# Optimization experiments

Measured on AMD Instinct MI355X. Metric: run time of the kernel, lower is better.

The kernel has to match this reference:

```python
import jax, jax.numpy as jnp
import numpy as np

B, S, HID = 1, 2048, 4096
NH, NKV, HD = 32, 8, 128
N_REP = NH // NKV
SCALING = HD ** -0.5
NEG_INF = jnp.float32(-jnp.inf)


def rotate_half(x):
    x1, x2 = jnp.split(x, 2, axis=-1)
    return jnp.concatenate((-x2, x1), axis=-1)


def setup_inputs() -> dict:
    key = jax.random.key(0)
    ks = jax.random.split(key, 8)
    hidden_states = jax.random.normal(ks[0], (B, S, HID), dtype=jnp.float32)
    # RoPE tables (uniform stand-ins; real cos/sin come from rotary embedding)
    pos = jnp.arange(S, dtype=jnp.float32)[:, None]
    inv_freq = 1.0 / (10000.0 ** (jnp.arange(0, HD, 2, dtype=jnp.float32) / HD))
    ang = pos * inv_freq[None, :]              # [S, HD/2]
    emb = jnp.concatenate([ang, ang], axis=-1)  # [S, HD]
    cos = jnp.cos(emb)[None].repeat(B, axis=0)  # [B, S, HD]
    sin = jnp.sin(emb)[None].repeat(B, axis=0)
    # HF-style additive causal mask: 0 on/below diagonal, -inf above
    tril = jnp.tril(jnp.ones((S, S), dtype=bool))
    attention_mask = jnp.where(tril, 0.0, NEG_INF).astype(jnp.float32)[None, None]  # [B,1,S,S]
    scale = 0.02
    q_w = jax.random.normal(ks[1], (HID, HID), dtype=jnp.float32) * scale
    k_w = jax.random.normal(ks[2], (NKV * HD, HID), dtype=jnp.float32) * scale
    v_w = jax.random.normal(ks[3], (NKV * HD, HID), dtype=jnp.float32) * scale
    o_w = jax.random.normal(ks[4], (HID, HID), dtype=jnp.float32) * scale
    return {"hidden_states": hidden_states, "cos": cos, "sin": sin,
            "attention_mask": attention_mask, "q_w": q_w, "k_w": k_w,
            "v_w": v_w, "o_w": o_w}


def reference(hidden_states, cos, sin, attention_mask, q_w, k_w, v_w, o_w):
    b, s, _ = hidden_states.shape
    # projections -> [B, H, S, D]
    q = (hidden_states @ q_w.T).reshape(b, s, NH, HD).transpose(0, 2, 1, 3)
    k = (hidden_states @ k_w.T).reshape(b, s, NKV, HD).transpose(0, 2, 1, 3)
    v = (hidden_states @ v_w.T).reshape(b, s, NKV, HD).transpose(0, 2, 1, 3)
    # RoPE (unsqueeze_dim=1)
    cos_u = cos[:, None, :, :]
    sin_u = sin[:, None, :, :]
    q = q * cos_u + rotate_half(q) * sin_u
    k = k * cos_u + rotate_half(k) * sin_u
    # repeat_kv (interleave each kv head n_rep times)
    k = jnp.repeat(k, N_REP, axis=1)
    v = jnp.repeat(v, N_REP, axis=1)
    attn = jnp.einsum("bhqd,bhkd->bhqk", q, k)
    # gen_mask: 0 -> 1, -inf -> 0 (passthrough otherwise)
    m = attention_mask
    mask01 = jnp.where(m == 0, 1.0, jnp.where(jnp.isneginf(m), 0.0, m))
    attn = attn * mask01
    causal = m[:, :, :, : k.shape[-2]]
    attn = (attn + causal) * SCALING
    probs = jax.nn.softmax(attn.astype(jnp.float32), axis=-1).astype(q.dtype)
    # dropout p=attention_dropout=0.0 in eval -> identity
    ctx = jnp.einsum("bhqk,bhkd->bhqd", probs, v)  # [B,H,S,D]
    out = ctx.transpose(0, 2, 1, 3).reshape(b, s, -1) @ o_w.T
    return out
```

## Files before the change

### kernel.cpp

```cpp
#include <hip/hip_runtime.h>


typedef __attribute__((ext_vector_type(8))) short bf16x8;
typedef __attribute__((ext_vector_type(4))) float f32x4;
typedef __attribute__((ext_vector_type(4))) unsigned short u16x4;

#define S_LEN 2048
#define HID 4096
#define NH 32
#define NKV 8
#define HD 128
#define KVDIM 1024
#define SCALING 0.08838834764831845f

__device__ inline unsigned short f2bf(float f) {
  unsigned u = __builtin_bit_cast(unsigned, f);
  u = (u + 0x7FFFu + ((u >> 16) & 1u)) >> 16;
  return (unsigned short)u;
}
__device__ inline unsigned short f2bf_fast(float f) {
  unsigned u = __builtin_bit_cast(unsigned, f);
  return (unsigned short)((u + 0x8000u) >> 16);
}
__device__ inline float bf2f(unsigned short h) {
  unsigned u = ((unsigned)h) << 16;
  return __builtin_bit_cast(float, u);
}

__device__ inline void gload_lds16(const unsigned short* g, unsigned short* l) {
  __builtin_amdgcn_global_load_lds(
      (const __attribute__((address_space(1))) void*)g,
      (__attribute__((address_space(3))) void*)l, 16, 0, 0);
}

#define SZ_HS (8388608u)
#define SZ_QW (16777216u)
#define SZ_KW (4194304u)
#define B0 SZ_HS
#define B1 (B0 + SZ_QW)
#define B2 (B1 + SZ_KW)
#define B3 (B2 + SZ_KW)
#define B4 (B3 + SZ_QW)

__global__ void cvt_all(const float* __restrict__ s0,
                        const float* __restrict__ s1,
                        const float* __restrict__ s2,
                        const float* __restrict__ s3,
                        const float* __restrict__ s4,
                        unsigned short* __restrict__ dst) {
  size_t i = ((size_t)blockIdx.x * blockDim.x + threadIdx.x) * 4;
  const float* src;
  size_t off;
  if (i < B0)      { src = s0; off = i; }
  else if (i < B1) { src = s1; off = i - B0; }
  else if (i < B2) { src = s2; off = i - B1; }
  else if (i < B3) { src = s3; off = i - B2; }
  else             { src = s4; off = i - B3; }
  f32x4 v = *(const f32x4*)(src + off);
  u16x4 o;
#pragma unroll
  for (int r = 0; r < 4; ++r) o[r] = f2bf(v[r]);
  *(u16x4*)(dst + i) = o;
}

__global__ __launch_bounds__(256, 3) void gemm_qkv(
    const unsigned short* __restrict__ A, const unsigned short* __restrict__ Bq_,
    const unsigned short* __restrict__ Bk_, const unsigned short* __restrict__ Bv_,
    unsigned short* __restrict__ Cq, unsigned short* __restrict__ Ck,
    unsigned short* __restrict__ Cvt) {
  __shared__ unsigned short As[2][128 * 32];
  __shared__ unsigned short Bs[2][128 * 32];
  const int K = HID;
  const int tid = threadIdx.x;
  const int lane = tid & 63;
  const int wave = tid >> 6;
  const int orig = blockIdx.y * gridDim.x + blockIdx.x;
  const int xcd = orig & 7, seq = orig >> 3;
  const int xt = xcd * ((int)gridDim.x >> 3) + (seq >> 4);
  const int yt = seq & 15;
  const int m0 = yt * 128;
  const int wr = wave >> 1, wc = wave & 1;
  const int lrow = lane & 15, lg = lane >> 4;

  const unsigned short* Bsel;
  if (xt < 32)      Bsel = Bq_ + (size_t)(xt * 128) * K;
  else if (xt < 40) Bsel = Bk_ + (size_t)((xt - 32) * 128) * K;
  else              Bsel = Bv_ + (size_t)((xt - 40) * 128) * K;

  const f32x4 zero = {0.f, 0.f, 0.f, 0.f};
  f32x4 acc[4][4];
#pragma unroll
  for (int i = 0; i < 4; ++i)
#pragma unroll
    for (int j = 0; j < 4; ++j) acc[i][j] = zero;

  const int r0s = tid >> 2, c0s = (tid & 3) * 8;
  const int r1s = (tid + 256) >> 2, c1s = ((tid + 256) & 3) * 8;
  const unsigned short* Ag0 = A + (size_t)(m0 + r0s) * K + c0s;
  const unsigned short* Ag1 = A + (size_t)(m0 + r1s) * K + c1s;
  const unsigned short* Bg0 = Bsel + (size_t)r0s * K + c0s;
  const unsigned short* Bg1 = Bsel + (size_t)r1s * K + c1s;
  unsigned short* Al0[2] = {&As[0][tid * 8], &As[1][tid * 8]};
  unsigned short* Al1[2] = {&As[0][(tid + 256) * 8], &As[1][(tid + 256) * 8]};
  unsigned short* Bl0[2] = {&Bs[0][tid * 8], &Bs[1][tid * 8]};
  unsigned short* Bl1[2] = {&Bs[0][(tid + 256) * 8], &Bs[1][(tid + 256) * 8]};

#define QKV_STAGE(buf, koff)                                                  \
  {                                                                           \
    gload_lds16(Ag0 + (koff), Al0[buf]);                                      \
    gload_lds16(Ag1 + (koff), Al1[buf]);                                      \
    gload_lds16(Bg0 + (koff), Bl0[buf]);                                      \
    gload_lds16(Bg1 + (koff), Bl1[buf]);                                      \
  }

  QKV_STAGE(0, 0);
  __syncthreads();
  int cur = 0;
  const int NT = K >> 5;
  for (int kt = 0; kt < NT; ++kt) {
    if (kt + 1 < NT) QKV_STAGE(cur ^ 1, (kt + 1) * 32);
    bf16x8 af[4], bq[4];
#pragma unroll
    for (int i = 0; i < 4; ++i) {
      af[i] = *(const bf16x8*)(&As[cur][(wr * 64 + i * 16 + lrow) * 32 + lg * 8]);
      bq[i] = *(const bf16x8*)(&Bs[cur][(wc * 64 + i * 16 + lrow) * 32 + lg * 8]);
    }
#pragma unroll
    for (int i = 0; i < 4; ++i)
#pragma unroll
      for (int j = 0; j < 4; ++j)
        acc[i][j] = __builtin_amdgcn_mfma_f32_16x16x32_bf16(af[i], bq[j],
                                                            acc[i][j], 0, 0, 0);
    __syncthreads();
    cur ^= 1;
  }
#undef QKV_STAGE

  if (xt < 32) {
    const int n0 = xt * 128;
#pragma unroll
    for (int i = 0; i < 4; ++i)
#pragma unroll
      for (int j = 0; j < 4; ++j) {
        const int mm = m0 + wr * 64 + i * 16 + lg * 4;
        const int nn = n0 + wc * 64 + j * 16 + lrow;
#pragma unroll
        for (int r = 0; r < 4; ++r)
          Cq[(size_t)(mm + r) * HID + nn] = f2bf(acc[i][j][r]);
      }
  } else if (xt < 40) {
    const int n0 = (xt - 32) * 128;
#pragma unroll
    for (int i = 0; i < 4; ++i)
#pragma unroll
      for (int j = 0; j < 4; ++j) {
        const int mm = m0 + wr * 64 + i * 16 + lg * 4;
        const int nn = n0 + wc * 64 + j * 16 + lrow;
#pragma unroll
        for (int r = 0; r < 4; ++r)
          Ck[(size_t)(mm + r) * KVDIM + nn] = f2bf(acc[i][j][r]);
      }
  } else {
    const int n0 = (xt - 40) * 128;
#pragma unroll
    for (int i = 0; i < 4; ++i)
#pragma unroll
      for (int j = 0; j < 4; ++j) {
        const int mm = m0 + wr * 64 + i * 16 + lg * 4;
        const int nn = n0 + wc * 64 + j * 16 + lrow;
        u16x4 pk;
#pragma unroll
        for (int r = 0; r < 4; ++r) pk[r] = f2bf(acc[i][j][r]);
        *(u16x4*)(Cvt + (size_t)nn * S_LEN + mm) = pk;
      }
  }
}

#define GEMM_STAGE(Abase, Bbase, buf, koff)                                   \
  {                                                                           \
    _Pragma("unroll") for (int q = 0; q < 4; ++q)                             \
        gload_lds16(Abase + (size_t)(q * 32) * K + (koff), Asl[buf] + q * 2048); \
    _Pragma("unroll") for (int q = 0; q < 4; ++q)                             \
        gload_lds16(Bbase + (size_t)(q * 32) * K + (koff), Bsl[buf] + q * 2048); \
  }

#define GEMM_COMPUTE(cur)                                                     \
  {                                                                           \
    bf16x8 af[4][2], bq[4][2];                                                \
    const int r7 = lrow & 7;                                                  \
    _Pragma("unroll") for (int i = 0; i < 4; ++i) {                           \
      const int arow = wr * 64 + i * 16 + lrow;                               \
      const int brow = wc * 64 + i * 16 + lrow;                               \
      _Pragma("unroll") for (int ks = 0; ks < 2; ++ks) {                      \
        af[i][ks] = *(const bf16x8*)(As[cur] + arow * 64 +                    \
                                     (((ks * 4 + lg) ^ r7) * 8));             \
        bq[i][ks] = *(const bf16x8*)(Bs[cur] + brow * 64 +                    \
                                     (((ks * 4 + lg) ^ r7) * 8));             \
      }                                                                       \
    }                                                                         \
    _Pragma("unroll") for (int i = 0; i < 4; ++i)                             \
        _Pragma("unroll") for (int j = 0; j < 4; ++j) {                       \
      acc[i][j] = __builtin_amdgcn_mfma_f32_16x16x32_bf16(af[i][0], bq[j][0], \
                                                          acc[i][j], 0, 0, 0);\
      acc[i][j] = __builtin_amdgcn_mfma_f32_16x16x32_bf16(af[i][1], bq[j][1], \
                                                          acc[i][j], 0, 0, 0);\
    }                                                                         \
  }

__global__ __launch_bounds__(256, 2) void gemm_o(
    const unsigned short* __restrict__ A, const unsigned short* __restrict__ B,
    float* __restrict__ C) {
  __shared__ unsigned short As[2][128 * 64];
  __shared__ unsigned short Bs[2][128 * 64];
  const int K = HID;
  const int tid = threadIdx.x;
  const int lane = tid & 63;
  const int wave = tid >> 6;
  const int orig = blockIdx.y * gridDim.x + blockIdx.x;
  const int xcd = orig & 7, seq = orig >> 3;
  const int xt = xcd * ((int)gridDim.x >> 3) + (seq >> 4);
  const int yt = seq & 15;
  const int m0 = yt * 128;
  const int n0 = xt * 128;
  const int wr = wave >> 1, wc = wave & 1;
  const int lrow = lane & 15, lg = lane >> 4;

  const f32x4 zero = {0.f, 0.f, 0.f, 0.f};
  f32x4 acc[4][4];
#pragma unroll
  for (int i = 0; i < 4; ++i)
#pragma unroll
    for (int j = 0; j < 4; ++j) acc[i][j] = zero;

  const int srow = tid >> 3;
  const int scol = ((tid & 7) ^ (srow & 7)) * 8;
  const unsigned short* Agb = A + (size_t)(m0 + srow) * K + scol;
  const unsigned short* Bgb = B + (size_t)(n0 + srow) * K + scol;
  unsigned short* Asl[2] = {As[0] + tid * 8, As[1] + tid * 8};
  unsigned short* Bsl[2] = {Bs[0] + tid * 8, Bs[1] + tid * 8};

  GEMM_STAGE(Agb, Bgb, 0, 0);
  __syncthreads();
  int cur = 0;
  const int NT = K / 64;
  for (int kt = 0; kt < NT; ++kt) {
    if (kt + 1 < NT) GEMM_STAGE(Agb, Bgb, cur ^ 1, (kt + 1) * 64);
    GEMM_COMPUTE(cur);
    __syncthreads();
    cur ^= 1;
  }

#pragma unroll
  for (int i = 0; i < 4; ++i)
#pragma unroll
    for (int j = 0; j < 4; ++j) {
      const int mm = m0 + wr * 64 + i * 16 + lg * 4;
      const int nn = n0 + wc * 64 + j * 16 + lrow;
#pragma unroll
      for (int r = 0; r < 4; ++r)
        C[(size_t)(mm + r) * HID + nn] = acc[i][j][r];
    }
}

__global__ void rope_qk(unsigned short* __restrict__ q,
                        unsigned short* __restrict__ k,
                        const float* __restrict__ cosb,
                        const float* __restrict__ sinb) {
  const int s = blockIdx.x;
  const int t = threadIdx.x;
  unsigned short* x;
  int h, d4, rowstride;
  if (t < 512) { x = q; rowstride = HID;   h = t >> 4;        d4 = t & 15; }
  else         { x = k; rowstride = KVDIM; h = (t - 512) >> 4; d4 = (t - 512) & 15; }
  const int d = d4 * 4;
  const f32x4 c = *(const f32x4*)(cosb + s * 128 + d);
  const f32x4 sn = *(const f32x4*)(sinb + s * 128 + d);
  unsigned short* base = x + (size_t)s * rowstride + h * 128;
  u16x4 lo = *(u16x4*)(base + d);
  u16x4 hi = *(u16x4*)(base + d + 64);
  u16x4 olo, ohi;
#pragma unroll
  for (int r = 0; r < 4; ++r) {
    float lf = bf2f(lo[r]), hf = bf2f(hi[r]);
    olo[r] = f2bf(lf * c[r] - hf * sn[r]);
    ohi[r] = f2bf(hf * c[r] + lf * sn[r]);
  }
  *(u16x4*)(base + d) = olo;
  *(u16x4*)(base + d + 64) = ohi;
}

__global__ __launch_bounds__(256, 2) void attn_kernel(
    const unsigned short* __restrict__ Q, const unsigned short* __restrict__ Kc,
    const unsigned short* __restrict__ Vt, unsigned short* __restrict__ ctx) {
  __shared__ unsigned short Ks[64 * 128];
  __shared__ unsigned short Vs[128 * 64];
  __shared__ unsigned short Ps[4][32 * 72];
  const int tid = threadIdx.x;
  const int lane = tid & 63;
  const int wave = tid >> 6;
  const int h = blockIdx.x;
  const int hk = h >> 2;
  const int yl = (int)gridDim.y - 1 - blockIdx.y;
  const int r0 = yl * 128 + wave * 32;
  const int lrow = lane & 15, lg = lane >> 4;

  bf16x8 aq[2][4];
#pragma unroll
  for (int i = 0; i < 2; ++i) {
    const unsigned short* qb =
        Q + (size_t)(r0 + i * 16 + lrow) * HID + h * HD + lg * 8;
#pragma unroll
    for (int kk = 0; kk < 4; ++kk) aq[i][kk] = *(const bf16x8*)(qb + kk * 32);
  }

  const f32x4 zero = {0.f, 0.f, 0.f, 0.f};
  f32x4 o[2][8];
#pragma unroll
  for (int i = 0; i < 2; ++i)
#pragma unroll
    for (int t = 0; t < 8; ++t) o[i][t] = zero;
  f32x4 l_acc[2] = {zero, zero};
  float m_i[2][4];
#pragma unroll
  for (int i = 0; i < 2; ++i)
#pragma unroll
    for (int r = 0; r < 4; ++r) m_i[i][r] = -1e30f;

  const short onebf = (short)0x3F80;
  const bf16x8 onesf = {onebf, onebf, onebf, onebf, onebf, onebf, onebf, onebf};

  const unsigned short* Kg[4];
  const unsigned short* Vg[4];
  unsigned short* Kl[4];
  unsigned short* Vl[4];
#pragma unroll
  for (int qq = 0; qq < 4; ++qq) {
    const int slot = tid + 256 * qq;
    {
      const int row = slot >> 4, ch = slot & 15;
      Kg[qq] = Kc + (size_t)row * KVDIM + hk * HD + ((ch ^ (row & 7)) * 8);
      Kl[qq] = Ks + slot * 8;
    }
    {
      const int row = slot >> 3, ch = slot & 7;
      Vg[qq] = Vt + ((size_t)hk * HD + row) * S_LEN + ((ch ^ (row & 7)) * 8);
      Vl[qq] = Vs + slot * 8;
    }
  }
  unsigned short* pw = &Ps[wave][0];

  const int kend = yl * 128 + 128;
  for (int k0 = 0; k0 < kend; k0 += 64) {
#pragma unroll
    for (int qq = 0; qq < 4; ++qq) gload_lds16(Kg[qq] + (size_t)k0 * KVDIM, Kl[qq]);
#pragma unroll
    for (int qq = 0; qq < 4; ++qq) gload_lds16(Vg[qq] + k0, Vl[qq]);
    __syncthreads();

    if (k0 <= r0 + 31) {
      f32x4 sacc[2][4];
#pragma unroll
      for (int i = 0; i < 2; ++i)
#pragma unroll
        for (int c = 0; c < 4; ++c) sacc[i][c] = zero;
#pragma unroll
      for (int c = 0; c < 4; ++c) {
        const int krow = c * 16 + lrow;
        bf16x8 bk[4];
#pragma unroll
        for (int kk = 0; kk < 4; ++kk)
          bk[kk] = *(const bf16x8*)(Ks + krow * 128 +
                                    (((kk * 4 + lg) ^ (krow & 7)) * 8));
#pragma unroll
        for (int i = 0; i < 2; ++i)
#pragma unroll
          for (int kk = 0; kk < 4; ++kk)
            sacc[i][c] = __builtin_amdgcn_mfma_f32_16x16x32_bf16(
                aq[i][kk], bk[kk], sacc[i][c], 0, 0, 0);
      }
      const bool full = (k0 + 63 <= r0);
#pragma unroll
      for (int i = 0; i < 2; ++i)
#pragma unroll
        for (int c = 0; c < 4; ++c)
#pragma unroll
          for (int r = 0; r < 4; ++r) {
            float v = sacc[i][c][r] * SCALING;
            if (!full) {
              const int row = r0 + i * 16 + lg * 4 + r;
              const int col = k0 + c * 16 + lrow;
              v = (col <= row) ? v : -1e30f;
            }
            sacc[i][c][r] = v;
          }
      float tm[2][4];
#pragma unroll
      for (int i = 0; i < 2; ++i)
#pragma unroll
        for (int r = 0; r < 4; ++r)
          tm[i][r] = fmaxf(fmaxf(sacc[i][0][r], sacc[i][1][r]),
                           fmaxf(sacc[i][2][r], sacc[i][3][r]));
#pragma unroll
      for (int mm = 1; mm < 16; mm <<= 1)
#pragma unroll
        for (int i = 0; i < 2; ++i)
#pragma unroll
          for (int r = 0; r < 4; ++r)
            tm[i][r] = fmaxf(tm[i][r], __shfl_xor(tm[i][r], mm, 64));
      bool grow = false;
#pragma unroll
      for (int i = 0; i < 2; ++i)
#pragma unroll
        for (int r = 0; r < 4; ++r) grow |= (tm[i][r] > m_i[i][r] + 8.0f);
      if (__any(grow)) {
        float sc[2][4];
#pragma unroll
        for (int i = 0; i < 2; ++i)
#pragma unroll
          for (int r = 0; r < 4; ++r) {
            const float mn = fmaxf(m_i[i][r], tm[i][r]);
            sc[i][r] = __expf(m_i[i][r] - mn);
            m_i[i][r] = mn;
          }
#pragma unroll
        for (int i = 0; i < 2; ++i) {
#pragma unroll
          for (int t = 0; t < 8; ++t)
#pragma unroll
            for (int r = 0; r < 4; ++r) o[i][t][r] *= sc[i][r];
#pragma unroll
          for (int r = 0; r < 4; ++r) l_acc[i][r] *= sc[i][r];
        }
      }
#pragma unroll
      for (int i = 0; i < 2; ++i)
#pragma unroll
        for (int c = 0; c < 4; ++c)
#pragma unroll
          for (int r = 0; r < 4; ++r)
            pw[(i * 16 + lg * 4 + r) * 72 + c * 16 + lrow] =
                f2bf_fast(__expf(sacc[i][c][r] - m_i[i][r]));
      bf16x8 pa[2][2];
#pragma unroll
      for (int i = 0; i < 2; ++i)
#pragma unroll
        for (int ks = 0; ks < 2; ++ks)
          pa[i][ks] =
              *(const bf16x8*)(pw + (i * 16 + lrow) * 72 + ks * 32 + lg * 8);
#pragma unroll
      for (int i = 0; i < 2; ++i)
#pragma unroll
        for (int ks = 0; ks < 2; ++ks)
          l_acc[i] = __builtin_amdgcn_mfma_f32_16x16x32_bf16(pa[i][ks], onesf,
                                                             l_acc[i], 0, 0, 0);
#pragma unroll
      for (int t = 0; t < 8; ++t) {
        const int vrow = t * 16 + lrow;
#pragma unroll
        for (int ks = 0; ks < 2; ++ks) {
          bf16x8 bv = *(const bf16x8*)(Vs + vrow * 64 +
                                       (((ks * 4 + lg) ^ (vrow & 7)) * 8));
#pragma unroll
          for (int i = 0; i < 2; ++i)
            o[i][t] = __builtin_amdgcn_mfma_f32_16x16x32_bf16(pa[i][ks], bv,
                                                              o[i][t], 0, 0, 0);
        }
      }
    }
    __syncthreads();
  }
  float inv[2][4];
#pragma unroll
  for (int i = 0; i < 2; ++i)
#pragma unroll
    for (int r = 0; r < 4; ++r) inv[i][r] = 1.f / l_acc[i][r];
#pragma unroll
  for (int i = 0; i < 2; ++i)
#pragma unroll
    for (int t = 0; t < 8; ++t)
#pragma unroll
      for (int r = 0; r < 4; ++r)
        ctx[(size_t)(r0 + i * 16 + lg * 4 + r) * HID + h * HD + t * 16 + lrow] =
            f2bf(o[i][t][r] * inv[i][r]);
}

extern "C" void kernel_launch(void* const* d_in, const int* in_sizes, int n_in,
                              void* d_out, int out_size, void* d_ws,
                              size_t ws_size, hipStream_t stream) {
  (void)in_sizes; (void)n_in; (void)out_size; (void)ws_size;
  const float* hs   = (const float*)d_in[0];
  const float* cosb = (const float*)d_in[1];
  const float* sinb = (const float*)d_in[2];
  const float* qw = (const float*)d_in[4];
  const float* kw = (const float*)d_in[5];
  const float* vw = (const float*)d_in[6];
  const float* ow = (const float*)d_in[7];
  float* out = (float*)d_out;

  unsigned short* ws = (unsigned short*)d_ws;
  unsigned short* hs_b = ws;
  unsigned short* qw_b = hs_b + SZ_HS;
  unsigned short* kw_b = qw_b + SZ_QW;
  unsigned short* vw_b = kw_b + SZ_KW;
  unsigned short* ow_b = vw_b + SZ_KW;
  unsigned short* q_b  = ow_b + SZ_QW;
  unsigned short* k_b  = q_b + SZ_HS;
  unsigned short* vt_b = k_b + (size_t)S_LEN * KVDIM;
  unsigned short* ctx_b = vt_b + (size_t)KVDIM * S_LEN;

  cvt_all<<<B4 / 1024, 256, 0, stream>>>(hs, qw, kw, vw, ow, hs_b);

  gemm_qkv<<<dim3(48, 16), 256, 0, stream>>>(hs_b, qw_b, kw_b, vw_b,
                                             q_b, k_b, vt_b);

  rope_qk<<<S_LEN, 640, 0, stream>>>(q_b, k_b, cosb, sinb);

  attn_kernel<<<dim3(NH, S_LEN / 128), 256, 0, stream>>>(q_b, k_b, vt_b, ctx_b);

  gemm_o<<<dim3(32, 16), 256, 0, stream>>>(ctx_b, ow_b, out);
}
```

Baseline: 348.2 us.

## Double-buffer K tiles in attention, read V from global, shrink O-proj K tile

The attention kernel now double-buffers K tiles in LDS so the next K tile loads while the current one is computed. V is no longer staged through LDS and is read directly from global memory, which frees LDS for the extra K buffer. The output-projection GEMM moves from a K-step of 64 to 32, halving its LDS footprint, and both kernels raise launch bounds to 3 blocks per CU for occupancy. The risks are higher global-load latency on the V path, since V is now read redundantly by each wave without LDS reuse, and twice as many loop iterations and barriers in the GEMM. The GEMM's LDS reads also drop the XOR swizzle, which may cause bank conflicts.

```diff
diff --git a/kernel.cpp b/kernel.cpp
--- a/kernel.cpp
+++ b/kernel.cpp
@@ -176,42 +176,11 @@
   }
 }
 
-#define GEMM_STAGE(Abase, Bbase, buf, koff)                                   \
-  {                                                                           \
-    _Pragma("unroll") for (int q = 0; q < 4; ++q)                             \
-        gload_lds16(Abase + (size_t)(q * 32) * K + (koff), Asl[buf] + q * 2048); \
-    _Pragma("unroll") for (int q = 0; q < 4; ++q)                             \
-        gload_lds16(Bbase + (size_t)(q * 32) * K + (koff), Bsl[buf] + q * 2048); \
-  }
-
-#define GEMM_COMPUTE(cur)                                                     \
-  {                                                                           \
-    bf16x8 af[4][2], bq[4][2];                                                \
-    const int r7 = lrow & 7;                                                  \
-    _Pragma("unroll") for (int i = 0; i < 4; ++i) {                           \
-      const int arow = wr * 64 + i * 16 + lrow;                               \
-      const int brow = wc * 64 + i * 16 + lrow;                               \
-      _Pragma("unroll") for (int ks = 0; ks < 2; ++ks) {                      \
-        af[i][ks] = *(const bf16x8*)(As[cur] + arow * 64 +                    \
-                                     (((ks * 4 + lg) ^ r7) * 8));             \
-        bq[i][ks] = *(const bf16x8*)(Bs[cur] + brow * 64 +                    \
-                                     (((ks * 4 + lg) ^ r7) * 8));             \
-      }                                                                       \
-    }                                                                         \
-    _Pragma("unroll") for (int i = 0; i < 4; ++i)                             \
-        _Pragma("unroll") for (int j = 0; j < 4; ++j) {                       \
-      acc[i][j] = __builtin_amdgcn_mfma_f32_16x16x32_bf16(af[i][0], bq[j][0], \
-                                                          acc[i][j], 0, 0, 0);\
-      acc[i][j] = __builtin_amdgcn_mfma_f32_16x16x32_bf16(af[i][1], bq[j][1], \
-                                                          acc[i][j], 0, 0, 0);\
-    }                                                                         \
-  }
-
-__global__ __launch_bounds__(256, 2) void gemm_o(
+__global__ __launch_bounds__(256, 3) void gemm_o(
     const unsigned short* __restrict__ A, const unsigned short* __restrict__ B,
     float* __restrict__ C) {
-  __shared__ unsigned short As[2][128 * 64];
-  __shared__ unsigned short Bs[2][128 * 64];
+  __shared__ unsigned short As[2][128 * 32];
+  __shared__ unsigned short Bs[2][128 * 32];
   const int K = HID;
   const int tid = threadIdx.x;
   const int lane = tid & 63;
@@ -232,23 +201,47 @@
 #pragma unroll
     for (int j = 0; j < 4; ++j) acc[i][j] = zero;
 
-  const int srow = tid >> 3;
-  const int scol = ((tid & 7) ^ (srow & 7)) * 8;
-  const unsigned short* Agb = A + (size_t)(m0 + srow) * K + scol;
-  const unsigned short* Bgb = B + (size_t)(n0 + srow) * K + scol;
-  unsigned short* Asl[2] = {As[0] + tid * 8, As[1] + tid * 8};
-  unsigned short* Bsl[2] = {Bs[0] + tid * 8, Bs[1] + tid * 8};
-
-  GEMM_STAGE(Agb, Bgb, 0, 0);
+  const int r0s = tid >> 2, c0s = (tid & 3) * 8;
+  const int r1s = (tid + 256) >> 2, c1s = ((tid + 256) & 3) * 8;
+  const unsigned short* Ag0 = A + (size_t)(m0 + r0s) * K + c0s;
+  const unsigned short* Ag1 = A + (size_t)(m0 + r1s) * K + c1s;
+  const unsigned short* Bg0 = B + (size_t)(n0 + r0s) * K + c0s;
+  const unsigned short* Bg1 = B + (size_t)(n0 + r1s) * K + c1s;
+  unsigned short* Al0[2] = {&As[0][tid * 8], &As[1][tid * 8]};
+  unsigned short* Al1[2] = {&As[0][(tid + 256) * 8], &As[1][(tid + 256) * 8]};
+  unsigned short* Bl0[2] = {&Bs[0][tid * 8], &Bs[1][tid * 8]};
+  unsigned short* Bl1[2] = {&Bs[0][(tid + 256) * 8], &Bs[1][(tid + 256) * 8]};
+
+#define O_STAGE(buf, koff)                                                    \
+  {                                                                           \
+    gload_lds16(Ag0 + (koff), Al0[buf]);                                      \
+    gload_lds16(Ag1 + (koff), Al1[buf]);                                      \
+    gload_lds16(Bg0 + (koff), Bl0[buf]);                                      \
+    gload_lds16(Bg1 + (koff), Bl1[buf]);                                      \
+  }
+
+  O_STAGE(0, 0);
   __syncthreads();
   int cur = 0;
-  const int NT = K / 64;
+  const int NT = K >> 5;
   for (int kt = 0; kt < NT; ++kt) {
-    if (kt + 1 < NT) GEMM_STAGE(Agb, Bgb, cur ^ 1, (kt + 1) * 64);
-    GEMM_COMPUTE(cur);
+    if (kt + 1 < NT) O_STAGE(cur ^ 1, (kt + 1) * 32);
+    bf16x8 af[4], bq[4];
+#pragma unroll
+    for (int i = 0; i < 4; ++i) {
+      af[i] = *(const bf16x8*)(&As[cur][(wr * 64 + i * 16 + lrow) * 32 + lg * 8]);
+      bq[i] = *(const bf16x8*)(&Bs[cur][(wc * 64 + i * 16 + lrow) * 32 + lg * 8]);
+    }
+#pragma unroll
+    for (int i = 0; i < 4; ++i)
+#pragma unroll
+      for (int j = 0; j < 4; ++j)
+        acc[i][j] = __builtin_amdgcn_mfma_f32_16x16x32_bf16(af[i], bq[j],
+                                                            acc[i][j], 0, 0, 0);
     __syncthreads();
     cur ^= 1;
   }
+#undef O_STAGE
 
 #pragma unroll
   for (int i = 0; i < 4; ++i)
@@ -289,11 +282,10 @@
   *(u16x4*)(base + d + 64) = ohi;
 }
 
-__global__ __launch_bounds__(256, 2) void attn_kernel(
+__global__ __launch_bounds__(256, 3) void attn_kernel(
     const unsigned short* __restrict__ Q, const unsigned short* __restrict__ Kc,
     const unsigned short* __restrict__ Vt, unsigned short* __restrict__ ctx) {
-  __shared__ unsigned short Ks[64 * 128];
-  __shared__ unsigned short Vs[128 * 64];
+  __shared__ unsigned short Ks[2][64 * 128];
   __shared__ unsigned short Ps[4][32 * 72];
   const int tid = threadIdx.x;
   const int lane = tid & 63;
@@ -330,32 +322,30 @@
   const bf16x8 onesf = {onebf, onebf, onebf, onebf, onebf, onebf, onebf, onebf};
 
   const unsigned short* Kg[4];
-  const unsigned short* Vg[4];
-  unsigned short* Kl[4];
-  unsigned short* Vl[4];
+  int Koff[4];
 #pragma unroll
   for (int qq = 0; qq < 4; ++qq) {
     const int slot = tid + 256 * qq;
-    {
-      const int row = slot >> 4, ch = slot & 15;
-      Kg[qq] = Kc + (size_t)row * KVDIM + hk * HD + ((ch ^ (row & 7)) * 8);
-      Kl[qq] = Ks + slot * 8;
-    }
-    {
-      const int row = slot >> 3, ch = slot & 7;
-      Vg[qq] = Vt + ((size_t)hk * HD + row) * S_LEN + ((ch ^ (row & 7)) * 8);
-      Vl[qq] = Vs + slot * 8;
-    }
-  }
+    const int row = slot >> 4, ch = slot & 15;
+    Kg[qq] = Kc + (size_t)row * KVDIM + hk * HD + ((ch ^ (row & 7)) * 8);
+    Koff[qq] = slot * 8;
+  }
+  const unsigned short* vbase =
+      Vt + ((size_t)hk * HD + lrow) * S_LEN + lg * 8;
   unsigned short* pw = &Ps[wave][0];
+
+#pragma unroll
+  for (int qq = 0; qq < 4; ++qq) gload_lds16(Kg[qq], &Ks[0][Koff[qq]]);
+  __syncthreads();
 
   const int kend = yl * 128 + 128;
   for (int k0 = 0; k0 < kend; k0 += 64) {
-#pragma unroll
-    for (int qq = 0; qq < 4; ++qq) gload_lds16(Kg[qq] + (size_t)k0 * KVDIM, Kl[qq]);
-#pragma unroll
-    for (int qq = 0; qq < 4; ++qq) gload_lds16(Vg[qq] + k0, Vl[qq]);
-    __syncthreads();
+    const int cur = (k0 >> 6) & 1;
+    if (k0 + 64 < kend) {
+#pragma unroll
+      for (int qq = 0; qq < 4; ++qq)
+        gload_lds16(Kg[qq] + (size_t)(k0 + 64) * KVDIM, &Ks[cur ^ 1][Koff[qq]]);
+    }
 
     if (k0 <= r0 + 31) {
       f32x4 sacc[2][4];
@@ -369,8 +359,8 @@
         bf16x8 bk[4];
 #pragma unroll
         for (int kk = 0; kk < 4; ++kk)
-          bk[kk] = *(const bf16x8*)(Ks + krow * 128 +
-                                    (((kk * 4 + lg) ^ (krow & 7)) * 8));
+          bk[kk] = *(const bf16x8*)(&Ks[cur][krow * 128 +
+                                            (((kk * 4 + lg) ^ (krow & 7)) * 8)]);
 #pragma unroll
         for (int i = 0; i < 2; ++i)
 #pragma unroll
@@ -455,11 +445,10 @@
                                                              l_acc[i], 0, 0, 0);
 #pragma unroll
       for (int t = 0; t < 8; ++t) {
-        const int vrow = t * 16 + lrow;
+        const unsigned short* vt0 = vbase + (size_t)(t * 16) * S_LEN + k0;
 #pragma unroll
         for (int ks = 0; ks < 2; ++ks) {
-          bf16x8 bv = *(const bf16x8*)(Vs + vrow * 64 +
-                                       (((ks * 4 + lg) ^ (vrow & 7)) * 8));
+          bf16x8 bv = *(const bf16x8*)(vt0 + ks * 32);
 #pragma unroll
           for (int i = 0; i < 2; ++i)
             o[i][t] = __builtin_amdgcn_mfma_f32_16x16x32_bf16(pa[i][ks], bv,
```

New measurement: 512.7 us. 47.2% more time.
